# Kernel tuning notes

Measured on AMD Instinct MI355X. Metric: run time of the kernel, lower is better.

The kernel has to match this reference:

```python
import jax, jax.numpy as jnp
import numpy as np

NHEAD = 16
D_MODEL = 1024
HEAD_DIM = D_MODEL // NHEAD


def setup_inputs() -> dict:
    key = jax.random.key(0)
    k1, k2, k3 = jax.random.split(key, 3)
    x = jax.random.normal(k1, (4, 2048, D_MODEL), dtype=jnp.float32)
    # lecun_normal-like scaling for stability
    w_qkv = jax.random.normal(k2, (D_MODEL, 3 * D_MODEL), dtype=jnp.float32) / np.sqrt(D_MODEL)
    w_out = jax.random.normal(k3, (D_MODEL, D_MODEL), dtype=jnp.float32) / np.sqrt(D_MODEL)
    return {"x": x, "w_qkv": w_qkv, "w_out": w_out}


def reference(x, w_qkv, w_out):
    # Fused QKV projection (self-attention: x_kv = x)
    qkv = x @ w_qkv  # [B, S, 3*D]
    q, k, v = jnp.split(qkv, 3, axis=-1)
    B, S = x.shape[0], x.shape[1]
    # [B, S, H, hd] -> [B, H, S, hd]
    q = jnp.moveaxis(q.reshape(B, S, NHEAD, HEAD_DIM), -2, -3)
    k = jnp.moveaxis(k.reshape(B, S, NHEAD, HEAD_DIM), -2, -3)
    v = jnp.moveaxis(v.reshape(B, S, NHEAD, HEAD_DIM), -2, -3)
    scale = 1.0 / jnp.sqrt(jnp.float32(HEAD_DIM))
    logits = jnp.einsum('bhqd,bhkd->bhqk', q, k) * scale
    weights = jax.nn.softmax(logits, axis=-1)
    out = jnp.einsum('bhqk,bhkd->bhqd', weights, v)  # [B, H, S, hd]
    out = jnp.moveaxis(out, -3, -2).reshape(B, S, D_MODEL)
    return out @ w_out
```

## Files before the change

### kernel.cpp

```cpp
#include <hip/hip_runtime.h>
#include <hip/hip_bf16.h>
#include <math.h>

#define D_MODEL 1024
#define NHEAD   16
#define HEAD_DIM 64
#define BATCH   4
#define SEQ     2048

typedef __attribute__((ext_vector_type(8))) short bf16x8;
typedef __attribute__((ext_vector_type(4))) float f32x4;
typedef __attribute__((ext_vector_type(16))) float f32x16;

__device__ inline ushort f2bf(float f) {
  __hip_bfloat16 h = __float2bfloat16(f);
  return *reinterpret_cast<ushort*>(&h);
}
__device__ inline uint pk2(float a, float b) {
  return (uint)f2bf(a) | ((uint)f2bf(b) << 16);
}
__device__ inline float bf2f(ushort u) {
  return __uint_as_float((uint)u << 16);
}
__device__ inline f32x16 zero16() {
  f32x16 z;
#pragma unroll
  for (int i = 0; i < 16; ++i) z[i] = 0.f;
  return z;
}
__device__ inline void gld_lds16(const ushort* g, ushort* l) {
  __builtin_amdgcn_global_load_lds(
      (const __attribute__((address_space(1))) void*)g,
      (__attribute__((address_space(3))) void*)l, 16, 0, 0);
}

__global__ __launch_bounds__(256) void fill_f32(float* __restrict__ p, int n, float v) {
  int i = blockIdx.x * 256 + threadIdx.x;
  if (i < n) p[i] = v;
}

__global__ __launch_bounds__(256) void cast_bf16(const float* __restrict__ in,
                                                 ushort* __restrict__ out, int n8) {
  int i = blockIdx.x * 256 + threadIdx.x;
  if (i >= n8) return;
  const float4* p = (const float4*)(in + i * 8);
  float4 a = p[0], b = p[1];
  uint4 o;
  o.x = pk2(a.x, a.y); o.y = pk2(a.z, a.w);
  o.z = pk2(b.x, b.y); o.w = pk2(b.z, b.w);
  ((uint4*)out)[i] = o;
}

__global__ __launch_bounds__(256) void transpose_f32_bf16(const float* __restrict__ in,
                                                          ushort* __restrict__ out,
                                                          int R, int C) {
  __shared__ float tile[32][33];
  int tx = threadIdx.x, ty = threadIdx.y;
  int c0 = blockIdx.x * 32, r0 = blockIdx.y * 32;
#pragma unroll
  for (int k = 0; k < 4; ++k)
    tile[ty + 8 * k][tx] = in[(size_t)(r0 + ty + 8 * k) * C + c0 + tx];
  __syncthreads();
#pragma unroll
  for (int k = 0; k < 4; ++k)
    out[(size_t)(c0 + ty + 8 * k) * R + r0 + tx] = f2bf(tile[tx][ty + 8 * k]);
}

template <typename OutT>
__global__ __launch_bounds__(256) void gemm_mfma(const ushort* __restrict__ A,
                                                 const ushort* __restrict__ BT,
                                                 OutT* __restrict__ C,
                                                 int M, int N, int K) {
  __shared__ ushort As[128 * 32];
  __shared__ ushort Bs[128 * 32];

  const int tid = threadIdx.x;
  const int w = tid >> 6, lane = tid & 63;
  const int quad = lane >> 4, l16 = lane & 15;

  int bx = blockIdx.x, by = blockIdx.y;
  {
    int nwg = gridDim.x * gridDim.y;
    if ((nwg & 7) == 0) {
      int bid = by * gridDim.x + bx;
      int chunk = nwg >> 3;
      bid = (bid & 7) * chunk + (bid >> 3);
      bx = bid % gridDim.x;
      by = bid / gridDim.x;
    }
  }
  const int m0 = by * 128, n0 = bx * 128;
  const int wm = (w & 1) * 64, wn = (w >> 1) * 64;

  f32x4 acc[4][4];
#pragma unroll
  for (int mt = 0; mt < 4; ++mt)
#pragma unroll
    for (int nt = 0; nt < 4; ++nt) acc[mt][nt] = (f32x4){0.f, 0.f, 0.f, 0.f};

  const int c0 = w * 64 + lane;
  const int r0a = c0 >> 2, k0a = (c0 & 3) * 8;
  const int c1 = 256 + c0;
  const int r1a = c1 >> 2, k1a = (c1 & 3) * 8;
  const ushort* a_src0 = A + (size_t)(m0 + r0a) * K + k0a;
  const ushort* a_src1 = A + (size_t)(m0 + r1a) * K + k1a;
  const ushort* b_src0 = BT + (size_t)(n0 + r0a) * K + k0a;
  const ushort* b_src1 = BT + (size_t)(n0 + r1a) * K + k1a;
  ushort* a_dst0 = As + (size_t)w * 512;
  ushort* a_dst1 = As + 2048 + (size_t)w * 512;
  ushort* b_dst0 = Bs + (size_t)w * 512;
  ushort* b_dst1 = Bs + 2048 + (size_t)w * 512;

  for (int k0 = 0; k0 < K; k0 += 32) {
    gld_lds16(a_src0 + k0, a_dst0);
    gld_lds16(a_src1 + k0, a_dst1);
    gld_lds16(b_src0 + k0, b_dst0);
    gld_lds16(b_src1 + k0, b_dst1);
    __syncthreads();

    bf16x8 af[4], bf[4];
#pragma unroll
    for (int mt = 0; mt < 4; ++mt)
      af[mt] = *(const bf16x8*)(As + (wm + mt * 16 + l16) * 32 + quad * 8);
#pragma unroll
    for (int nt = 0; nt < 4; ++nt)
      bf[nt] = *(const bf16x8*)(Bs + (wn + nt * 16 + l16) * 32 + quad * 8);
#pragma unroll
    for (int mt = 0; mt < 4; ++mt)
#pragma unroll
      for (int nt = 0; nt < 4; ++nt)
        acc[mt][nt] = __builtin_amdgcn_mfma_f32_16x16x32_bf16(af[mt], bf[nt], acc[mt][nt], 0, 0, 0);
    __syncthreads();
  }

#pragma unroll
  for (int mt = 0; mt < 4; ++mt) {
#pragma unroll
    for (int nt = 0; nt < 4; ++nt) {
#pragma unroll
      for (int r = 0; r < 4; ++r) {
        size_t idx = (size_t)(m0 + wm + mt * 16 + quad * 4 + r) * N + n0 + wn + nt * 16 + l16;
        if constexpr (sizeof(OutT) == 4) C[idx] = acc[mt][nt][r];
        else                             C[idx] = f2bf(acc[mt][nt][r]);
      }
    }
  }
}

#define KST 72
#define VST 72
__global__ __launch_bounds__(256, 4) void attn_mfma(const ushort* __restrict__ qkv,
                                                    ushort* __restrict__ attn_o) {
  __shared__ ushort Ks[64 * KST];
  __shared__ ushort VTs[64 * VST];

  const int tid = threadIdx.x;
  const int w = tid >> 6, lane = tid & 63;
  const int q32 = lane & 31, hi = lane >> 5;
  const int b = blockIdx.z, h = blockIdx.y, qb = blockIdx.x;
  const int q0 = qb * 128;

  const float qscale = 0.125f * 1.44269504088896f;
  bf16x8 qfrag[4];
  {
    const ushort* qrow = qkv + (size_t)(b * SEQ + q0 + w * 32 + q32) * 3072 + h * 64;
#pragma unroll
    for (int dd = 0; dd < 4; ++dd) {
      bf16x8 f = *(const bf16x8*)(qrow + dd * 16 + hi * 8);
#pragma unroll
      for (int j = 0; j < 8; ++j)
        f[j] = (short)f2bf(bf2f((ushort)f[j]) * qscale);
      qfrag[dd] = f;
    }
  }

  f32x16 oacc0 = zero16(), oacc1 = zero16(), lacc = zero16();

  bf16x8 ones;
#pragma unroll
  for (int j = 0; j < 8; ++j) ones[j] = (short)0x3F80;

  const int sr = tid >> 2, sc = tid & 3;
  const int kp = tid & 31, dg = tid >> 5;

  const size_t kstep = (size_t)64 * 3072;
  const ushort* kbase = qkv + (size_t)(b * SEQ + sr) * 3072 + 1024 + h * 64 + sc * 16;
  const ushort* vbase = qkv + (size_t)(b * SEQ + 2 * kp) * 3072 + 2048 + h * 64 + dg * 8;

  uint4 kreg0, kreg1, vreg0, vreg1;
  {
    const uint4* ks = (const uint4*)kbase;
    kreg0 = ks[0]; kreg1 = ks[1];
    vreg0 = *(const uint4*)vbase;
    vreg1 = *(const uint4*)(vbase + 3072);
  }

  for (int kt = 0; kt < SEQ / 64; ++kt) {
    {
      uint4* kdst = (uint4*)(Ks + sr * KST + sc * 16);
      kdst[0] = kreg0; kdst[1] = kreg1;
      const ushort* ae = (const ushort*)&vreg0;
      const ushort* ce = (const ushort*)&vreg1;
#pragma unroll
      for (int j = 0; j < 8; ++j)
        *(uint*)(VTs + (dg * 8 + j) * VST + 2 * kp) = (uint)ae[j] | ((uint)ce[j] << 16);
    }
    __syncthreads();

    bf16x8 pa[4];
#pragma unroll
    for (int kblk = 0; kblk < 2; ++kblk) {
      f32x16 sacc = zero16();
      __builtin_amdgcn_s_setprio(1);
#pragma unroll
      for (int dd = 0; dd < 4; ++dd) {
        bf16x8 kf = *(const bf16x8*)(Ks + (kblk * 32 + q32) * KST + dd * 16 + hi * 8);
        sacc = __builtin_amdgcn_mfma_f32_32x32x16_bf16(kf, qfrag[dd], sacc, 0, 0, 0);
      }
      __builtin_amdgcn_s_setprio(0);

      uint d0[4], d1[4];
#pragma unroll
      for (int p = 0; p < 4; ++p) {
        d0[p] = pk2(exp2f(sacc[4 * p + 0]), exp2f(sacc[4 * p + 1]));
        d1[p] = pk2(exp2f(sacc[4 * p + 2]), exp2f(sacc[4 * p + 3]));
      }
#pragma unroll
      for (int k2 = 0; k2 < 2; ++k2) {
        uint A0 = d0[2 * k2], B0 = d0[2 * k2 + 1];
        uint A1 = d1[2 * k2], B1 = d1[2 * k2 + 1];
        asm("v_permlane32_swap_b32 %0, %1" : "+v"(A0), "+v"(B0));
        asm("v_permlane32_swap_b32 %0, %1" : "+v"(A1), "+v"(B1));
        uint4 fr = {A0, A1, B0, B1};
        pa[kblk * 2 + k2] = *(bf16x8*)&fr;
        lacc = __builtin_amdgcn_mfma_f32_32x32x16_bf16(pa[kblk * 2 + k2], ones, lacc, 0, 0, 0);
      }
    }

    {
      int ktn = (kt + 1) & (SEQ / 64 - 1);
      const uint4* ks = (const uint4*)(kbase + ktn * kstep);
      kreg0 = ks[0]; kreg1 = ks[1];
      vreg0 = *(const uint4*)(vbase + ktn * kstep);
      vreg1 = *(const uint4*)(vbase + ktn * kstep + 3072);
    }

    __builtin_amdgcn_s_setprio(1);
#pragma unroll
    for (int kb2 = 0; kb2 < 4; ++kb2) {
      bf16x8 vf0 = *(const bf16x8*)(VTs + (q32)*VST + kb2 * 16 + hi * 8);
      bf16x8 vf1 = *(const bf16x8*)(VTs + (32 + q32) * VST + kb2 * 16 + hi * 8);
      oacc0 = __builtin_amdgcn_mfma_f32_32x32x16_bf16(pa[kb2], vf0, oacc0, 0, 0, 0);
      oacc1 = __builtin_amdgcn_mfma_f32_32x32x16_bf16(pa[kb2], vf1, oacc1, 0, 0, 0);
    }
    __builtin_amdgcn_s_setprio(0);
    __syncthreads();
  }

#pragma unroll
  for (int p = 0; p < 4; ++p) {
#pragma unroll
    for (int r = 0; r < 4; ++r) {
      int qrow = r + 8 * p + 4 * hi;
      float linv = 1.0f / lacc[4 * p + r];
      ushort* orow = attn_o + (size_t)(b * SEQ + q0 + w * 32 + qrow) * 1024 + h * 64 + q32;
      orow[0]  = f2bf(oacc0[4 * p + r] * linv);
      orow[32] = f2bf(oacc1[4 * p + r] * linv);
    }
  }
}

extern "C" void kernel_launch(void* const* d_in, const int* in_sizes, int n_in,
                              void* d_out, int out_size, void* d_ws, size_t ws_size,
                              hipStream_t stream) {
  bool ok_n  = (n_in == 3);
  bool ok_s0 = ok_n && (in_sizes[0] == 4 * 2048 * 1024);
  bool ok_s1 = ok_n && (in_sizes[1] == 1024 * 3072);
  bool ok_s2 = ok_n && (in_sizes[2] == 1024 * 1024);
  bool ok_o  = (out_size == 4 * 2048 * 1024);
  bool ok_w  = (ws_size >= (size_t)8192 * 3072 * 4);
  if (!(ok_n && ok_s0 && ok_s1 && ok_s2 && ok_o && ok_w)) {
    float c = 64.0f + 1.0f * ok_n + 2.0f * ok_s0 + 4.0f * ok_s1 +
              8.0f * ok_s2 + 16.0f * ok_o + 32.0f * ok_w;
    fill_f32<<<(out_size + 255) / 256, 256, 0, stream>>>((float*)d_out, out_size, c);
    return;
  }

  const float* x     = (const float*)d_in[0];
  const float* w_qkv = (const float*)d_in[1];
  const float* w_out = (const float*)d_in[2];

  char* ws = (char*)d_ws;
  ushort* qkv    = (ushort*)ws;
  ushort* xb     = (ushort*)(ws + (size_t)48 * 1024 * 1024);
  ushort* attn_o = (ushort*)(ws + (size_t)64 * 1024 * 1024);
  ushort* wqkvT  = (ushort*)(ws + (size_t)80 * 1024 * 1024);
  ushort* woutT  = (ushort*)(ws + (size_t)86 * 1024 * 1024);

  cast_bf16<<<dim3(8192 * 1024 / 8 / 256), dim3(256), 0, stream>>>(x, xb, 8192 * 1024 / 8);
  transpose_f32_bf16<<<dim3(3072 / 32, 1024 / 32), dim3(32, 8), 0, stream>>>(w_qkv, wqkvT, 1024, 3072);
  transpose_f32_bf16<<<dim3(1024 / 32, 1024 / 32), dim3(32, 8), 0, stream>>>(w_out, woutT, 1024, 1024);

  gemm_mfma<ushort><<<dim3(3072 / 128, 8192 / 128), dim3(256), 0, stream>>>(
      xb, wqkvT, qkv, 8192, 3072, 1024);

  attn_mfma<<<dim3(SEQ / 128, NHEAD, BATCH), dim3(256), 0, stream>>>(qkv, attn_o);

  gemm_mfma<float><<<dim3(1024 / 128, 8192 / 128), dim3(256), 0, stream>>>(
      attn_o, woutT, (float*)d_out, 8192, 1024, 1024);
}
```

Before: 307.6 us.

## Double-buffer K/V tiles in LDS and remap attention blocks per XCD

The attention kernel now keeps two LDS buffers for K and V^T. Each iteration writes the next tile into the alternate buffer after its compute, which leaves one barrier per iteration instead of two. The launch becomes a 1D grid of 1024 blocks. Blocks are remapped so that all query blocks of one (batch, head) pair fall on the same XCD, which should improve L2 reuse of K/V. LDS use doubles, which may limit occupancy, and the mapping relies on round-robin assignment of blocks to XCDs.

```diff
diff --git a/kernel.cpp b/kernel.cpp
--- a/kernel.cpp
+++ b/kernel.cpp
@@ -149,15 +149,22 @@
 
 #define KST 72
 #define VST 72
+#define NT  (SEQ / 64)
 __global__ __launch_bounds__(256, 4) void attn_mfma(const ushort* __restrict__ qkv,
                                                     ushort* __restrict__ attn_o) {
-  __shared__ ushort Ks[64 * KST];
-  __shared__ ushort VTs[64 * VST];
+  __shared__ ushort Ks[2][64 * KST];
+  __shared__ ushort VTs[2][64 * VST];
 
   const int tid = threadIdx.x;
   const int w = tid >> 6, lane = tid & 63;
   const int q32 = lane & 31, hi = lane >> 5;
-  const int b = blockIdx.z, h = blockIdx.y, qb = blockIdx.x;
+
+  const int f = blockIdx.x;
+  const int xcd = f & 7;
+  const int j = f >> 3;
+  const int qb = j & 15;
+  const int hb = ((j >> 4) << 3) | xcd;
+  const int h = hb & 15, b = hb >> 4;
   const int q0 = qb * 128;
 
   const float qscale = 0.125f * 1.44269504088896f;
@@ -166,11 +173,11 @@
     const ushort* qrow = qkv + (size_t)(b * SEQ + q0 + w * 32 + q32) * 3072 + h * 64;
 #pragma unroll
     for (int dd = 0; dd < 4; ++dd) {
-      bf16x8 f = *(const bf16x8*)(qrow + dd * 16 + hi * 8);
-#pragma unroll
-      for (int j = 0; j < 8; ++j)
-        f[j] = (short)f2bf(bf2f((ushort)f[j]) * qscale);
-      qfrag[dd] = f;
+      bf16x8 fq = *(const bf16x8*)(qrow + dd * 16 + hi * 8);
+#pragma unroll
+      for (int jj = 0; jj < 8; ++jj)
+        fq[jj] = (short)f2bf(bf2f((ushort)fq[jj]) * qscale);
+      qfrag[dd] = fq;
     }
   }
 
@@ -178,7 +185,7 @@
 
   bf16x8 ones;
 #pragma unroll
-  for (int j = 0; j < 8; ++j) ones[j] = (short)0x3F80;
+  for (int jj = 0; jj < 8; ++jj) ones[jj] = (short)0x3F80;
 
   const int sr = tid >> 2, sc = tid & 3;
   const int kp = tid & 31, dg = tid >> 5;
@@ -193,19 +200,25 @@
     kreg0 = ks[0]; kreg1 = ks[1];
     vreg0 = *(const uint4*)vbase;
     vreg1 = *(const uint4*)(vbase + 3072);
-  }
-
-  for (int kt = 0; kt < SEQ / 64; ++kt) {
-    {
-      uint4* kdst = (uint4*)(Ks + sr * KST + sc * 16);
-      kdst[0] = kreg0; kdst[1] = kreg1;
-      const ushort* ae = (const ushort*)&vreg0;
-      const ushort* ce = (const ushort*)&vreg1;
-#pragma unroll
-      for (int j = 0; j < 8; ++j)
-        *(uint*)(VTs + (dg * 8 + j) * VST + 2 * kp) = (uint)ae[j] | ((uint)ce[j] << 16);
-    }
+    uint4* kdst = (uint4*)(Ks[0] + sr * KST + sc * 16);
+    kdst[0] = kreg0; kdst[1] = kreg1;
+    const ushort* ae = (const ushort*)&vreg0;
+    const ushort* ce = (const ushort*)&vreg1;
+#pragma unroll
+    for (int jj = 0; jj < 8; ++jj)
+      *(uint*)(VTs[0] + (dg * 8 + jj) * VST + 2 * kp) = (uint)ae[jj] | ((uint)ce[jj] << 16);
+  }
+
+  for (int kt = 0; kt < NT; ++kt) {
+    const int cur = kt & 1;
     __syncthreads();
+
+    if (kt + 1 < NT) {
+      const uint4* ks = (const uint4*)(kbase + (size_t)(kt + 1) * kstep);
+      kreg0 = ks[0]; kreg1 = ks[1];
+      vreg0 = *(const uint4*)(vbase + (size_t)(kt + 1) * kstep);
+      vreg1 = *(const uint4*)(vbase + (size_t)(kt + 1) * kstep + 3072);
+    }
 
     bf16x8 pa[4];
 #pragma unroll
@@ -214,7 +227,7 @@
       __builtin_amdgcn_s_setprio(1);
 #pragma unroll
       for (int dd = 0; dd < 4; ++dd) {
-        bf16x8 kf = *(const bf16x8*)(Ks + (kblk * 32 + q32) * KST + dd * 16 + hi * 8);
+        bf16x8 kf = *(const bf16x8*)(Ks[cur] + (kblk * 32 + q32) * KST + dd * 16 + hi * 8);
         sacc = __builtin_amdgcn_mfma_f32_32x32x16_bf16(kf, qfrag[dd], sacc, 0, 0, 0);
       }
       __builtin_amdgcn_s_setprio(0);
@@ -237,24 +250,25 @@
       }
     }
 
-    {
-      int ktn = (kt + 1) & (SEQ / 64 - 1);
-      const uint4* ks = (const uint4*)(kbase + ktn * kstep);
-      kreg0 = ks[0]; kreg1 = ks[1];
-      vreg0 = *(const uint4*)(vbase + ktn * kstep);
-      vreg1 = *(const uint4*)(vbase + ktn * kstep + 3072);
-    }
-
     __builtin_amdgcn_s_setprio(1);
 #pragma unroll
     for (int kb2 = 0; kb2 < 4; ++kb2) {
-      bf16x8 vf0 = *(const bf16x8*)(VTs + (q32)*VST + kb2 * 16 + hi * 8);
-      bf16x8 vf1 = *(const bf16x8*)(VTs + (32 + q32) * VST + kb2 * 16 + hi * 8);
+      bf16x8 vf0 = *(const bf16x8*)(VTs[cur] + (q32)*VST + kb2 * 16 + hi * 8);
+      bf16x8 vf1 = *(const bf16x8*)(VTs[cur] + (32 + q32) * VST + kb2 * 16 + hi * 8);
       oacc0 = __builtin_amdgcn_mfma_f32_32x32x16_bf16(pa[kb2], vf0, oacc0, 0, 0, 0);
       oacc1 = __builtin_amdgcn_mfma_f32_32x32x16_bf16(pa[kb2], vf1, oacc1, 0, 0, 0);
     }
     __builtin_amdgcn_s_setprio(0);
-    __syncthreads();
+
+    if (kt + 1 < NT) {
+      uint4* kdst = (uint4*)(Ks[cur ^ 1] + sr * KST + sc * 16);
+      kdst[0] = kreg0; kdst[1] = kreg1;
+      const ushort* ae = (const ushort*)&vreg0;
+      const ushort* ce = (const ushort*)&vreg1;
+#pragma unroll
+      for (int jj = 0; jj < 8; ++jj)
+        *(uint*)(VTs[cur ^ 1] + (dg * 8 + jj) * VST + 2 * kp) = (uint)ae[jj] | ((uint)ce[jj] << 16);
+    }
   }
 
 #pragma unroll
@@ -304,7 +318,7 @@
   gemm_mfma<ushort><<<dim3(3072 / 128, 8192 / 128), dim3(256), 0, stream>>>(
       xb, wqkvT, qkv, 8192, 3072, 1024);
 
-  attn_mfma<<<dim3(SEQ / 128, NHEAD, BATCH), dim3(256), 0, stream>>>(qkv, attn_o);
+  attn_mfma<<<dim3(1024), dim3(256), 0, stream>>>(qkv, attn_o);
 
   gemm_mfma<float><<<dim3(1024 / 128, 8192 / 128), dim3(256), 0, stream>>>(
       attn_o, woutT, (float*)d_out, 8192, 1024, 1024);
```

Result: no change. 303.8 us (-1.2%).
